# Kernel optimization log

Measured on AMD Instinct MI355X. Metric: run time of the kernel, lower is better.

## Reference

```python
import jax, jax.numpy as jnp
import numpy as np

B, S, D = 1024, 256, 128  # batch, seq_len, emb_dim; concat feat = 4*D = 512
H1, H2 = 256, 64          # att_hidden_size tail; att_hidden_size = [4*D, H1, H2]


def setup_inputs() -> dict:
    key = jax.random.key(0)
    ks = jax.random.split(key, 8)
    queries = jax.random.normal(ks[0], (B, D), dtype=jnp.float32)
    keys = jax.random.normal(ks[1], (B, S, D), dtype=jnp.float32)
    keys_length = jax.random.randint(ks[2], (B,), 1, S + 1)  # in [1, S]
    W1 = jax.random.normal(ks[3], (4 * D, H1), dtype=jnp.float32) * (1.0 / np.sqrt(4 * D))
    b1 = jnp.zeros((H1,), dtype=jnp.float32)
    W2 = jax.random.normal(ks[4], (H1, H2), dtype=jnp.float32) * (1.0 / np.sqrt(H1))
    b2 = jnp.zeros((H2,), dtype=jnp.float32)
    Wd = jax.random.normal(ks[5], (H2, 1), dtype=jnp.float32) * (1.0 / np.sqrt(H2))
    bd = jnp.zeros((1,), dtype=jnp.float32)
    return {"queries": queries, "keys": keys, "keys_length": keys_length,
            "W1": W1, "b1": b1, "W2": W2, "b2": b2, "Wd": Wd, "bd": bd}


def reference(queries, keys, keys_length, W1, b1, W2, b2, Wd, bd):
    # broadcast query across sequence: [B, S, D]
    q = jnp.broadcast_to(queries[:, None, :], keys.shape)
    feat = jnp.concatenate([q, keys, q - keys, q * keys], axis=-1)
    # att MLP (sigmoid after each layer, as in MLPLayers)
    h = jax.nn.sigmoid(jnp.einsum('bsf,fh->bsh', feat, W1) + b1)
    h = jax.nn.sigmoid(jnp.einsum('bsh,hk->bsk', h, W2) + b2)
    score = (jnp.einsum('bsk,ko->bso', h, Wd) + bd)[..., 0]  # [B, S]
    # mask: positions >= keys_length are invalid (mask_mat = arange(S))
    mask = jnp.arange(S)[None, :] >= keys_length[:, None]
    score = jnp.where(mask, -jnp.inf, score)  # softmax_stag=True -> -inf fill
    score = score / jnp.sqrt(jnp.float32(D))
    w = jax.nn.softmax(score, axis=1)  # [B, S]
    # return_seq_weight=False -> weighted sum over keys: [B, 1, D]
    out = jnp.einsum('bs,bsd->bd', w, keys)[:, None, :]
    return out
```

## Files before the change

### kernel.cpp

```cpp
#include <hip/hip_runtime.h>


typedef unsigned short u16;
typedef unsigned int u32;
typedef short bf16x8 __attribute__((ext_vector_type(8)));
typedef float f32x4 __attribute__((ext_vector_type(4)));

#define NBATCH 1024
#define SLEN 256
#define DD 128
#define NH1 256
#define NH2 64

#define WS_WBCT  0
#define WS_WDT   65536
#define WS_W2T   131072
#define WS_WDS   163840
#define WS_WSUM  165888
#define WS_BIAS1 296960

#define L_KBUF   0
#define L_H1     16384
#define L_SCORES 32768
#define L_BIAS   33792
#define L_B2     34816
#define L_WD     35072
#define L_WPART  35344
#define L_RED4   35856
#define L_SIZE   35920

__device__ __forceinline__ u16 f2bf_rne(float f){
  union { float f; unsigned u; } v; v.f = f;
  unsigned r = v.u + 0x7fffu + ((v.u >> 16) & 1u);
  return (u16)(r >> 16);
}
__device__ __forceinline__ u32 pack_trunc(float a, float b){
  return (__float_as_uint(a) >> 16) | (__float_as_uint(b) & 0xffff0000u);
}
__device__ __forceinline__ float b2fl(short s){
  return __uint_as_float(((u32)(u16)s) << 16);
}
__device__ __forceinline__ int swz(int byte){
  return byte ^ (((byte >> 9) & 7) << 4);
}
__device__ __forceinline__ int swzk(int byte){
  return byte ^ (((byte >> 8) & 7) << 4);
}
__device__ __forceinline__ float fsigmoid(float x){
  return __builtin_amdgcn_rcpf(1.f + __expf(-x));
}
__device__ __forceinline__ void barrier_lds(){
  asm volatile("s_waitcnt lgkmcnt(0)" ::: "memory");
  __builtin_amdgcn_s_barrier();
  __builtin_amdgcn_sched_barrier(0);
}

__global__ void prep_weights(const float* __restrict__ W1, const float* __restrict__ W2,
                             const float* __restrict__ Wd, const float* __restrict__ bd,
                             u16* __restrict__ WbcT, u16* __restrict__ WdT,
                             u16* __restrict__ W2T, float* __restrict__ WdS,
                             float* __restrict__ Wsum){
  int n = blockIdx.x;
  int k = threadIdx.x;
  if (k < DD){
    WbcT[n * DD + k] = f2bf_rne(W1[(128 + k) * NH1 + n] - W1[(256 + k) * NH1 + n]);
    WdT [n * DD + k] = f2bf_rne(W1[(384 + k) * NH1 + n]);
    Wsum[k * NH1 + n] = W1[k * NH1 + n] + W1[(256 + k) * NH1 + n];
  }
  if (n < NH2) W2T[n * 256 + k] = f2bf_rne(W2[k * NH2 + n]);
  if (n == 0 && k < NH2) WdS[k] = Wd[k];
  if (n == 0 && k == NH2) WdS[NH2] = bd[0];
}

__global__ void prep_bias(const float* __restrict__ q, const float* __restrict__ Wsum,
                          const float* __restrict__ b1, float* __restrict__ bias1){
  __shared__ float qsh[DD];
  int b = blockIdx.x, j = threadIdx.x;
  if (j < DD) qsh[j] = q[b * DD + j];
  __syncthreads();
  float acc = b1[j];
  #pragma unroll 8
  for (int d = 0; d < DD; ++d)
    acc += qsh[d] * Wsum[d * NH1 + j];
  bias1[b * NH1 + j] = acc;
}

__global__ __launch_bounds__(512, 4)
void seqatt_main(const float* __restrict__ queries, const float* __restrict__ keys,
                 const int* __restrict__ keys_length,
                 const u16* __restrict__ WbcT, const u16* __restrict__ WdT,
                 const u16* __restrict__ W2Tg,
                 const float* __restrict__ WdS, const float* __restrict__ bias1g,
                 const float* __restrict__ b2g, float* __restrict__ out)
{
  __shared__ alignas(16) char smem[L_SIZE];
  float* scores = (float*)(smem + L_SCORES);
  float* bias1s = (float*)(smem + L_BIAS);
  float* b2s    = (float*)(smem + L_B2);
  float* wds    = (float*)(smem + L_WD);
  float* wpart  = (float*)(smem + L_WPART);
  float* red4   = (float*)(smem + L_RED4);

  const int b = blockIdx.x;
  const int tid = threadIdx.x;
  const int lane = tid & 63;
  const int wave = tid >> 6;
  const int l15 = lane & 15;
  const int g   = lane >> 4;
  const int r = tid >> 4, seg = tid & 15;

  if (tid < 256) bias1s[tid] = bias1g[b * NH1 + tid];
  if (tid < 64) b2s[tid] = b2g[tid];
  if (tid < 65) wds[tid] = WdS[tid];
  const int klen = keys_length[b];
  const float* kbb = keys + (long)b * SLEN * DD;

  float4 k0, k1;
#define ISSUE(t) do { const float* p_ = kbb + (((t) << 5) + r) * DD + (seg << 3); \
    k0 = *(const float4*)p_; k1 = *(const float4*)(p_ + 4); } while (0)
#define STORE(t) do { int bb_ = (((t) & 1) << 13) + (r << 8) + (seg << 4); \
    uint4 w_; \
    w_.x = pack_trunc(k0.x, k0.y); w_.y = pack_trunc(k0.z, k0.w); \
    w_.z = pack_trunc(k1.x, k1.y); w_.w = pack_trunc(k1.z, k1.w); \
    *(uint4*)(smem + swzk(bb_)) = w_; } while (0)

  ISSUE(0);

  bf16x8 bfrag[2][4];
  {
    const float* qb = queries + b * DD;
    #pragma unroll
    for (int nt = 0; nt < 2; ++nt){
      int n = (wave << 5) + (nt << 4) + l15;
      #pragma unroll
      for (int kk = 0; kk < 4; ++kk){
        int k0i = (g << 3) + (kk << 5);
        bf16x8 bc = *(const bf16x8*)(WbcT + n * DD + k0i);
        bf16x8 wd = *(const bf16x8*)(WdT  + n * DD + k0i);
        float4 q0 = *(const float4*)(qb + k0i);
        float4 q1 = *(const float4*)(qb + k0i + 4);
        float qa[8] = {q0.x, q0.y, q0.z, q0.w, q1.x, q1.y, q1.z, q1.w};
        union { u16 s[8]; bf16x8 v; } o;
        #pragma unroll
        for (int j = 0; j < 8; ++j)
          o.s[j] = f2bf_rne(fmaf(qa[j], b2fl(wd[j]), b2fl(bc[j])));
        bfrag[nt][kk] = o.v;
      }
    }
  }
  const int sh = wave >> 2;
  const int ob = (wave & 3) << 4;
  bf16x8 w2frag[8];
  #pragma unroll
  for (int kk = 0; kk < 8; ++kk)
    w2frag[kk] = *(const bf16x8*)(W2Tg + (ob + l15) * 256 + (kk << 5) + (g << 3));

  STORE(0);
  barrier_lds();

  const f32x4 fz = {0.f, 0.f, 0.f, 0.f};

  for (int st = 0; st < 8; ++st){
    const int s0 = st << 5;
    const int kb_base = (st & 1) << 13;

    if (st < 7) ISSUE(st + 1);

    f32x4 acc[2][2];
    #pragma unroll
    for (int mt = 0; mt < 2; ++mt)
      #pragma unroll
      for (int nt = 0; nt < 2; ++nt) acc[mt][nt] = fz;
    #pragma unroll
    for (int kk = 0; kk < 4; ++kk){
      bf16x8 af[2];
      #pragma unroll
      for (int mt = 0; mt < 2; ++mt)
        af[mt] = *(const bf16x8*)(smem + swzk(kb_base + (((mt << 4) + l15) << 8) + (kk << 6) + (g << 4)));
      #pragma unroll
      for (int mt = 0; mt < 2; ++mt)
        #pragma unroll
        for (int nt = 0; nt < 2; ++nt)
          acc[mt][nt] = __builtin_amdgcn_mfma_f32_16x16x32_bf16(bfrag[nt][kk], af[mt], acc[mt][nt], 0, 0, 0);
    }

    #pragma unroll
    for (int nt = 0; nt < 2; ++nt){
      float4 bia = *(const float4*)(bias1s + (wave << 5) + (nt << 4) + (g << 2));
      #pragma unroll
      for (int mt = 0; mt < 2; ++mt){
        float v0 = fsigmoid(acc[mt][nt][0] + bia.x);
        float v1 = fsigmoid(acc[mt][nt][1] + bia.y);
        float v2 = fsigmoid(acc[mt][nt][2] + bia.z);
        float v3 = fsigmoid(acc[mt][nt][3] + bia.w);
        uint2 p; p.x = pack_trunc(v0, v1); p.y = pack_trunc(v2, v3);
        int s = (mt << 4) + l15;
        int hb = (wave << 5) + (nt << 4) + (g << 2);
        *(uint2*)(smem + swz(L_H1 + (s << 9) + (hb << 1))) = p;
      }
    }
    barrier_lds();

    f32x4 acc2 = fz;
    #pragma unroll
    for (int kk = 0; kk < 8; ++kk){
      bf16x8 a2 = *(const bf16x8*)(smem + swz(L_H1 + (((sh << 4) + l15) << 9) + (kk << 6) + (g << 4)));
      acc2 = __builtin_amdgcn_mfma_f32_16x16x32_bf16(w2frag[kk], a2, acc2, 0, 0, 0);
    }

    {
      float pp = 0.f;
      #pragma unroll
      for (int i = 0; i < 4; ++i){
        int o = ob + (g << 2) + i;
        pp += fsigmoid(acc2[i] + b2s[o]) * wds[o];
      }
      pp += __shfl_xor(pp, 16); pp += __shfl_xor(pp, 32);
      if (lane < 16)
        wpart[((wave & 3) << 5) + (sh << 4) + l15] = pp;
    }

    if (st < 7) STORE(st + 1);

    barrier_lds();

    if (tid < 32){
      float v = wpart[tid] + wpart[32 + tid] + wpart[64 + tid] + wpart[96 + tid];
      int s = s0 + tid;
      scores[s] = (s < klen) ? (v + wds[64]) * 0.08838834764831845f : -1e30f;
    }
  }

  barrier_lds();

  {
    float v = (tid < 256) ? scores[tid] : -1e30f;
    float m = v;
    #pragma unroll
    for (int off = 32; off >= 1; off >>= 1) m = fmaxf(m, __shfl_xor(m, off));
    if (lane == 0) red4[wave] = m;
    __syncthreads();
    float mx = red4[0];
    #pragma unroll
    for (int w = 1; w < 8; ++w) mx = fmaxf(mx, red4[w]);
    float e = (tid < 256) ? __expf(v - mx) : 0.f;
    float ssum = e;
    #pragma unroll
    for (int off = 32; off >= 1; off >>= 1) ssum += __shfl_xor(ssum, off);
    if (lane == 0) red4[8 + wave] = ssum;
    __syncthreads();
    float tot = 0.f;
    #pragma unroll
    for (int w = 0; w < 8; ++w) tot += red4[8 + w];
    if (tid < 256) scores[tid] = e * __builtin_amdgcn_rcpf(tot);
    __syncthreads();
  }

  {
    float* red = (float*)smem;
    int d = tid & 127, q4 = tid >> 7;
    const float* kb = keys + ((long)b * SLEN + q4 * 64) * DD + d;
    const float* sc = scores + q4 * 64;
    float acc = 0.f;
    #pragma unroll 4
    for (int s2 = 0; s2 < 64; ++s2) acc += sc[s2] * kb[s2 * DD];
    red[tid] = acc;
    __syncthreads();
    if (tid < 128)
      out[b * DD + tid] = (red[tid] + red[128 + tid]) + (red[256 + tid] + red[384 + tid]);
  }
#undef ISSUE
#undef STORE
}

extern "C" void kernel_launch(void* const* d_in, const int* in_sizes, int n_in,
                              void* d_out, int out_size, void* d_ws, size_t ws_size,
                              hipStream_t stream) {
  const float* queries     = (const float*)d_in[0];
  const float* keys        = (const float*)d_in[1];
  const int*   keys_length = (const int*)d_in[2];
  const float* W1 = (const float*)d_in[3];
  const float* b1 = (const float*)d_in[4];
  const float* W2 = (const float*)d_in[5];
  const float* b2 = (const float*)d_in[6];
  const float* Wd = (const float*)d_in[7];
  const float* bd = (const float*)d_in[8];
  float* out = (float*)d_out;
  char* ws = (char*)d_ws;

  u16*   WbcT  = (u16*)(ws + WS_WBCT);
  u16*   WdT   = (u16*)(ws + WS_WDT);
  u16*   W2T   = (u16*)(ws + WS_W2T);
  float* WdS   = (float*)(ws + WS_WDS);
  float* Wsum  = (float*)(ws + WS_WSUM);
  float* bias1 = (float*)(ws + WS_BIAS1);

  prep_weights<<<dim3(256), dim3(256), 0, stream>>>(W1, W2, Wd, bd, WbcT, WdT, W2T, WdS, Wsum);
  prep_bias<<<dim3(NBATCH), dim3(256), 0, stream>>>(queries, Wsum, b1, bias1);
  seqatt_main<<<dim3(NBATCH), dim3(512), 0, stream>>>(queries, keys, keys_length,
                                                      WbcT, WdT, W2T, WdS, bias1, b2, out);
}
```

Baseline: 89.55 us.

## Fuse softmax-weighted key sum into streaming loop using LDS bf16 keys

Keeps three bf16 key tiles in LDS (triple buffering instead of double) so that each tile can be reused after its scores are computed. The weighted sum over keys is accumulated inside the main sequence loop, which removes the second global read of the keys. Softmax no longer subtracts the max: each score is exponentiated directly and the result is divided by the total at the end. The layer-2 MFMA chain is split into two independent accumulators to shorten the dependency chain. In exchange, the output now uses bf16-truncated keys, there is overflow risk if scores become large, and the extra LDS may lower occupancy.

```diff
diff --git a/kernel.cpp b/kernel.cpp
--- a/kernel.cpp
+++ b/kernel.cpp
@@ -20,14 +20,14 @@
 #define WS_BIAS1 296960
 
 #define L_KBUF   0
-#define L_H1     16384
-#define L_SCORES 32768
-#define L_BIAS   33792
-#define L_B2     34816
-#define L_WD     35072
-#define L_WPART  35344
-#define L_RED4   35856
-#define L_SIZE   35920
+#define L_H1     24576
+#define L_SCORES 40960
+#define L_BIAS   41984
+#define L_B2     43008
+#define L_WD     43264
+#define L_WPART  43536
+#define L_RED4   44048
+#define L_SIZE   44112
 
 __device__ __forceinline__ u16 f2bf_rne(float f){
   union { float f; unsigned u; } v; v.f = f;
@@ -108,21 +108,30 @@
   const int l15 = lane & 15;
   const int g   = lane >> 4;
   const int r = tid >> 4, seg = tid & 15;
+  const int dcol = tid & 127, so = (tid >> 7) << 3;
 
   if (tid < 256) bias1s[tid] = bias1g[b * NH1 + tid];
   if (tid < 64) b2s[tid] = b2g[tid];
   if (tid < 65) wds[tid] = WdS[tid];
   const int klen = keys_length[b];
   const float* kbb = keys + (long)b * SLEN * DD;
+  float out_acc = 0.f;
 
   float4 k0, k1;
 #define ISSUE(t) do { const float* p_ = kbb + (((t) << 5) + r) * DD + (seg << 3); \
     k0 = *(const float4*)p_; k1 = *(const float4*)(p_ + 4); } while (0)
-#define STORE(t) do { int bb_ = (((t) & 1) << 13) + (r << 8) + (seg << 4); \
+#define STORE(t) do { int bb_ = ((t) % 3) * 8192 + (r << 8) + (seg << 4); \
     uint4 w_; \
     w_.x = pack_trunc(k0.x, k0.y); w_.y = pack_trunc(k0.z, k0.w); \
     w_.z = pack_trunc(k1.x, k1.y); w_.w = pack_trunc(k1.z, k1.w); \
     *(uint4*)(smem + swzk(bb_)) = w_; } while (0)
+#define ACCUM(t) do { const int kb3_ = ((t) % 3) * 8192; \
+    _Pragma("unroll") \
+    for (int i_ = 0; i_ < 8; ++i_){ \
+      float w_ = scores[((t) << 5) + so + i_]; \
+      u16 kv_ = *(const u16*)(smem + kb3_ + ((so + i_) << 8) + ((dcol << 1) ^ (i_ << 4))); \
+      out_acc = fmaf(w_, b2fl((short)kv_), out_acc); \
+    } } while (0)
 
   ISSUE(0);
 
@@ -160,9 +169,9 @@
 
   const f32x4 fz = {0.f, 0.f, 0.f, 0.f};
 
+  #pragma unroll
   for (int st = 0; st < 8; ++st){
-    const int s0 = st << 5;
-    const int kb_base = (st & 1) << 13;
+    const int kb_base = (st % 3) * 8192;
 
     if (st < 7) ISSUE(st + 1);
 
@@ -201,11 +210,18 @@
     }
     barrier_lds();
 
-    f32x4 acc2 = fz;
-    #pragma unroll
-    for (int kk = 0; kk < 8; ++kk){
+    if (st > 0) ACCUM(st - 1);
+
+    f32x4 acc2a = fz, acc2b = fz;
+    #pragma unroll
+    for (int kk = 0; kk < 4; ++kk){
       bf16x8 a2 = *(const bf16x8*)(smem + swz(L_H1 + (((sh << 4) + l15) << 9) + (kk << 6) + (g << 4)));
-      acc2 = __builtin_amdgcn_mfma_f32_16x16x32_bf16(w2frag[kk], a2, acc2, 0, 0, 0);
+      acc2a = __builtin_amdgcn_mfma_f32_16x16x32_bf16(w2frag[kk], a2, acc2a, 0, 0, 0);
+    }
+    #pragma unroll
+    for (int kk = 4; kk < 8; ++kk){
+      bf16x8 a2 = *(const bf16x8*)(smem + swz(L_H1 + (((sh << 4) + l15) << 9) + (kk << 6) + (g << 4)));
+      acc2b = __builtin_amdgcn_mfma_f32_16x16x32_bf16(w2frag[kk], a2, acc2b, 0, 0, 0);
     }
 
     {
@@ -213,7 +229,7 @@
       #pragma unroll
       for (int i = 0; i < 4; ++i){
         int o = ob + (g << 2) + i;
-        pp += fsigmoid(acc2[i] + b2s[o]) * wds[o];
+        pp += fsigmoid((acc2a[i] + acc2b[i]) + b2s[o]) * wds[o];
       }
       pp += __shfl_xor(pp, 16); pp += __shfl_xor(pp, 32);
       if (lane < 16)
@@ -226,51 +242,37 @@
 
     if (tid < 32){
       float v = wpart[tid] + wpart[32 + tid] + wpart[64 + tid] + wpart[96 + tid];
-      int s = s0 + tid;
-      scores[s] = (s < klen) ? (v + wds[64]) * 0.08838834764831845f : -1e30f;
+      int s = (st << 5) + tid;
+      float sc = (v + wds[64]) * 0.08838834764831845f;
+      scores[s] = (s < klen) ? __expf(sc) : 0.f;
     }
   }
 
   barrier_lds();
-
+  ACCUM(7);
+
+  float tot;
   {
-    float v = (tid < 256) ? scores[tid] : -1e30f;
-    float m = v;
-    #pragma unroll
-    for (int off = 32; off >= 1; off >>= 1) m = fmaxf(m, __shfl_xor(m, off));
-    if (lane == 0) red4[wave] = m;
+    float v = (tid < 256) ? scores[tid] : 0.f;
+    #pragma unroll
+    for (int off = 32; off >= 1; off >>= 1) v += __shfl_xor(v, off);
+    if (lane == 0) red4[wave] = v;
     __syncthreads();
-    float mx = red4[0];
-    #pragma unroll
-    for (int w = 1; w < 8; ++w) mx = fmaxf(mx, red4[w]);
-    float e = (tid < 256) ? __expf(v - mx) : 0.f;
-    float ssum = e;
-    #pragma unroll
-    for (int off = 32; off >= 1; off >>= 1) ssum += __shfl_xor(ssum, off);
-    if (lane == 0) red4[8 + wave] = ssum;
-    __syncthreads();
-    float tot = 0.f;
-    #pragma unroll
-    for (int w = 0; w < 8; ++w) tot += red4[8 + w];
-    if (tid < 256) scores[tid] = e * __builtin_amdgcn_rcpf(tot);
-    __syncthreads();
+    tot = ((red4[0] + red4[1]) + (red4[2] + red4[3])) +
+          ((red4[4] + red4[5]) + (red4[6] + red4[7]));
   }
 
   {
     float* red = (float*)smem;
-    int d = tid & 127, q4 = tid >> 7;
-    const float* kb = keys + ((long)b * SLEN + q4 * 64) * DD + d;
-    const float* sc = scores + q4 * 64;
-    float acc = 0.f;
-    #pragma unroll 4
-    for (int s2 = 0; s2 < 64; ++s2) acc += sc[s2] * kb[s2 * DD];
-    red[tid] = acc;
+    red[tid] = out_acc;
     __syncthreads();
     if (tid < 128)
-      out[b * DD + tid] = (red[tid] + red[128 + tid]) + (red[256 + tid] + red[384 + tid]);
+      out[b * DD + tid] = ((red[tid] + red[128 + tid]) + (red[256 + tid] + red[384 + tid]))
+                          * __builtin_amdgcn_rcpf(tot);
   }
 #undef ISSUE
 #undef STORE
+#undef ACCUM
 }
 
 extern "C" void kernel_launch(void* const* d_in, const int* in_sizes, int n_in,
```

Measured after the change: 210.6 us. 2.35x slower.

## Fold log2e into weights, pad LDS rows instead of XOR swizzle, unroll stage loop

Applied to the files above, without the earlier changes.

Pre-scales W1, W2, the biases and the score scale by log2(e), so the sigmoids and the softmax can use exp2 directly and skip a multiply per exponent. XOR-swizzled LDS addressing is replaced by padded row strides (272 and 528 bytes) with precomputed base offsets. The stage loop is fully unrolled, and the second MFMA chain is split across two accumulators to shorten the dependency chain. This costs somewhat more LDS and code size, and the bf16 rounding of the pre-scaled weights shifts slightly.

```diff
diff --git a/kernel.cpp b/kernel.cpp
--- a/kernel.cpp
+++ b/kernel.cpp
@@ -11,6 +11,7 @@
 #define DD 128
 #define NH1 256
 #define NH2 64
+#define LOG2E 1.4426950408889634f
 
 #define WS_WBCT  0
 #define WS_WDT   65536
@@ -19,15 +20,17 @@
 #define WS_WSUM  165888
 #define WS_BIAS1 296960
 
-#define L_KBUF   0
-#define L_H1     16384
-#define L_SCORES 32768
-#define L_BIAS   33792
-#define L_B2     34816
-#define L_WD     35072
-#define L_WPART  35344
-#define L_RED4   35856
-#define L_SIZE   35920
+#define KROW     272
+#define KBUFSZ   8704
+#define H1ROW    528
+#define L_H1     17408
+#define L_BIAS   34304
+#define L_B2     35328
+#define L_WD     35584
+#define L_WPART  35856
+#define L_SCORES 36368
+#define L_RED4   37392
+#define L_SIZE   37456
 
 __device__ __forceinline__ u16 f2bf_rne(float f){
   union { float f; unsigned u; } v; v.f = f;
@@ -40,14 +43,8 @@
 __device__ __forceinline__ float b2fl(short s){
   return __uint_as_float(((u32)(u16)s) << 16);
 }
-__device__ __forceinline__ int swz(int byte){
-  return byte ^ (((byte >> 9) & 7) << 4);
-}
-__device__ __forceinline__ int swzk(int byte){
-  return byte ^ (((byte >> 8) & 7) << 4);
-}
-__device__ __forceinline__ float fsigmoid(float x){
-  return __builtin_amdgcn_rcpf(1.f + __expf(-x));
+__device__ __forceinline__ float fsig2(float x){
+  return __builtin_amdgcn_rcpf(1.f + exp2f(-x));
 }
 __device__ __forceinline__ void barrier_lds(){
   asm volatile("s_waitcnt lgkmcnt(0)" ::: "memory");
@@ -63,11 +60,11 @@
   int n = blockIdx.x;
   int k = threadIdx.x;
   if (k < DD){
-    WbcT[n * DD + k] = f2bf_rne(W1[(128 + k) * NH1 + n] - W1[(256 + k) * NH1 + n]);
-    WdT [n * DD + k] = f2bf_rne(W1[(384 + k) * NH1 + n]);
-    Wsum[k * NH1 + n] = W1[k * NH1 + n] + W1[(256 + k) * NH1 + n];
-  }
-  if (n < NH2) W2T[n * 256 + k] = f2bf_rne(W2[k * NH2 + n]);
+    WbcT[n * DD + k] = f2bf_rne((W1[(128 + k) * NH1 + n] - W1[(256 + k) * NH1 + n]) * LOG2E);
+    WdT [n * DD + k] = f2bf_rne(W1[(384 + k) * NH1 + n] * LOG2E);
+    Wsum[k * NH1 + n] = (W1[k * NH1 + n] + W1[(256 + k) * NH1 + n]) * LOG2E;
+  }
+  if (n < NH2) W2T[n * 256 + k] = f2bf_rne(W2[k * NH2 + n] * LOG2E);
   if (n == 0 && k < NH2) WdS[k] = Wd[k];
   if (n == 0 && k == NH2) WdS[NH2] = bd[0];
 }
@@ -78,7 +75,7 @@
   int b = blockIdx.x, j = threadIdx.x;
   if (j < DD) qsh[j] = q[b * DD + j];
   __syncthreads();
-  float acc = b1[j];
+  float acc = b1[j] * LOG2E;
   #pragma unroll 8
   for (int d = 0; d < DD; ++d)
     acc += qsh[d] * Wsum[d * NH1 + j];
@@ -94,11 +91,11 @@
                  const float* __restrict__ b2g, float* __restrict__ out)
 {
   __shared__ alignas(16) char smem[L_SIZE];
-  float* scores = (float*)(smem + L_SCORES);
   float* bias1s = (float*)(smem + L_BIAS);
   float* b2s    = (float*)(smem + L_B2);
   float* wds    = (float*)(smem + L_WD);
   float* wpart  = (float*)(smem + L_WPART);
+  float* scores = (float*)(smem + L_SCORES);
   float* red4   = (float*)(smem + L_RED4);
 
   const int b = blockIdx.x;
@@ -110,19 +107,23 @@
   const int r = tid >> 4, seg = tid & 15;
 
   if (tid < 256) bias1s[tid] = bias1g[b * NH1 + tid];
-  if (tid < 64) b2s[tid] = b2g[tid];
+  if (tid < 64) b2s[tid] = b2g[tid] * LOG2E;
   if (tid < 65) wds[tid] = WdS[tid];
   const int klen = keys_length[b];
   const float* kbb = keys + (long)b * SLEN * DD;
 
+  const int a1base = l15 * KROW + (g << 4);
+  const int hwbase = L_H1 + l15 * H1ROW + (((wave << 5) + (g << 2)) << 1);
+  const int stbase = r * KROW + (seg << 4);
+
   float4 k0, k1;
 #define ISSUE(t) do { const float* p_ = kbb + (((t) << 5) + r) * DD + (seg << 3); \
     k0 = *(const float4*)p_; k1 = *(const float4*)(p_ + 4); } while (0)
-#define STORE(t) do { int bb_ = (((t) & 1) << 13) + (r << 8) + (seg << 4); \
+#define STORE(t) do { \
     uint4 w_; \
     w_.x = pack_trunc(k0.x, k0.y); w_.y = pack_trunc(k0.z, k0.w); \
     w_.z = pack_trunc(k1.x, k1.y); w_.w = pack_trunc(k1.z, k1.w); \
-    *(uint4*)(smem + swzk(bb_)) = w_; } while (0)
+    *(uint4*)(smem + (((t) & 1) * KBUFSZ + stbase)) = w_; } while (0)
 
   ISSUE(0);
 
@@ -150,6 +151,7 @@
   }
   const int sh = wave >> 2;
   const int ob = (wave & 3) << 4;
+  const int a2base = L_H1 + ((sh << 4) + l15) * H1ROW + (g << 4);
   bf16x8 w2frag[8];
   #pragma unroll
   for (int kk = 0; kk < 8; ++kk)
@@ -160,9 +162,9 @@
 
   const f32x4 fz = {0.f, 0.f, 0.f, 0.f};
 
+  #pragma unroll
   for (int st = 0; st < 8; ++st){
-    const int s0 = st << 5;
-    const int kb_base = (st & 1) << 13;
+    const int kb_base = (st & 1) * KBUFSZ;
 
     if (st < 7) ISSUE(st + 1);
 
@@ -176,7 +178,7 @@
       bf16x8 af[2];
       #pragma unroll
       for (int mt = 0; mt < 2; ++mt)
-        af[mt] = *(const bf16x8*)(smem + swzk(kb_base + (((mt << 4) + l15) << 8) + (kk << 6) + (g << 4)));
+        af[mt] = *(const bf16x8*)(smem + (kb_base + a1base + mt * 4352 + (kk << 6)));
       #pragma unroll
       for (int mt = 0; mt < 2; ++mt)
         #pragma unroll
@@ -189,23 +191,26 @@
       float4 bia = *(const float4*)(bias1s + (wave << 5) + (nt << 4) + (g << 2));
       #pragma unroll
       for (int mt = 0; mt < 2; ++mt){
-        float v0 = fsigmoid(acc[mt][nt][0] + bia.x);
-        float v1 = fsigmoid(acc[mt][nt][1] + bia.y);
-        float v2 = fsigmoid(acc[mt][nt][2] + bia.z);
-        float v3 = fsigmoid(acc[mt][nt][3] + bia.w);
+        float v0 = fsig2(acc[mt][nt][0] + bia.x);
+        float v1 = fsig2(acc[mt][nt][1] + bia.y);
+        float v2 = fsig2(acc[mt][nt][2] + bia.z);
+        float v3 = fsig2(acc[mt][nt][3] + bia.w);
         uint2 p; p.x = pack_trunc(v0, v1); p.y = pack_trunc(v2, v3);
-        int s = (mt << 4) + l15;
-        int hb = (wave << 5) + (nt << 4) + (g << 2);
-        *(uint2*)(smem + swz(L_H1 + (s << 9) + (hb << 1))) = p;
+        *(uint2*)(smem + (hwbase + mt * 8448 + (nt << 5))) = p;
       }
     }
     barrier_lds();
 
-    f32x4 acc2 = fz;
-    #pragma unroll
-    for (int kk = 0; kk < 8; ++kk){
-      bf16x8 a2 = *(const bf16x8*)(smem + swz(L_H1 + (((sh << 4) + l15) << 9) + (kk << 6) + (g << 4)));
-      acc2 = __builtin_amdgcn_mfma_f32_16x16x32_bf16(w2frag[kk], a2, acc2, 0, 0, 0);
+    f32x4 acc2a = fz, acc2b = fz;
+    #pragma unroll
+    for (int kk = 0; kk < 4; ++kk){
+      bf16x8 a2 = *(const bf16x8*)(smem + (a2base + (kk << 6)));
+      acc2a = __builtin_amdgcn_mfma_f32_16x16x32_bf16(w2frag[kk], a2, acc2a, 0, 0, 0);
+    }
+    #pragma unroll
+    for (int kk = 4; kk < 8; ++kk){
+      bf16x8 a2 = *(const bf16x8*)(smem + (a2base + (kk << 6)));
+      acc2b = __builtin_amdgcn_mfma_f32_16x16x32_bf16(w2frag[kk], a2, acc2b, 0, 0, 0);
     }
 
     {
@@ -213,7 +218,7 @@
       #pragma unroll
       for (int i = 0; i < 4; ++i){
         int o = ob + (g << 2) + i;
-        pp += fsigmoid(acc2[i] + b2s[o]) * wds[o];
+        pp += fsig2((acc2a[i] + acc2b[i]) + b2s[o]) * wds[o];
       }
       pp += __shfl_xor(pp, 16); pp += __shfl_xor(pp, 32);
       if (lane < 16)
@@ -226,8 +231,9 @@
 
     if (tid < 32){
       float v = wpart[tid] + wpart[32 + tid] + wpart[64 + tid] + wpart[96 + tid];
-      int s = s0 + tid;
-      scores[s] = (s < klen) ? (v + wds[64]) * 0.08838834764831845f : -1e30f;
+      int s = (st << 5) + tid;
+      float sc = (v + wds[64]) * 0.12751744692290092f;
+      scores[s] = (s < klen) ? sc : -1e30f;
     }
   }
 
@@ -243,7 +249,7 @@
     float mx = red4[0];
     #pragma unroll
     for (int w = 1; w < 8; ++w) mx = fmaxf(mx, red4[w]);
-    float e = (tid < 256) ? __expf(v - mx) : 0.f;
+    float e = (tid < 256) ? exp2f(v - mx) : 0.f;
     float ssum = e;
     #pragma unroll
     for (int off = 32; off >= 1; off >>= 1) ssum += __shfl_xor(ssum, off);
```

New measurement: 101.9 us (median of 2 runs). +13.8%, slower.

## Triple-buffer keys and double-buffer H1/wpart to drop one barrier per step

Applied to the files above, without the earlier changes.

Keys staging in LDS goes from two to three rotating buffers, and the H1 activations and score partials are double-buffered. This lets the next tile's store and the previous step's score reduction move ahead of the layer-2 MMA, removing one block-wide barrier per sequence step. The layer-2 accumulation is also split into two independent accumulator chains to shorten the MFMA dependency chain. In exchange, LDS use grows from about 35 KB to about 61 KB per block, which may lower occupancy.

```diff
diff --git a/kernel.cpp b/kernel.cpp
--- a/kernel.cpp
+++ b/kernel.cpp
@@ -20,14 +20,14 @@
 #define WS_BIAS1 296960
 
 #define L_KBUF   0
-#define L_H1     16384
-#define L_SCORES 32768
-#define L_BIAS   33792
-#define L_B2     34816
-#define L_WD     35072
-#define L_WPART  35344
-#define L_RED4   35856
-#define L_SIZE   35920
+#define L_H1     24576
+#define L_SCORES 57344
+#define L_BIAS   58368
+#define L_B2     59392
+#define L_WD     59648
+#define L_WPART  59920
+#define L_RED4   60944
+#define L_SIZE   61008
 
 __device__ __forceinline__ u16 f2bf_rne(float f){
   union { float f; unsigned u; } v; v.f = f;
@@ -118,7 +118,7 @@
   float4 k0, k1;
 #define ISSUE(t) do { const float* p_ = kbb + (((t) << 5) + r) * DD + (seg << 3); \
     k0 = *(const float4*)p_; k1 = *(const float4*)(p_ + 4); } while (0)
-#define STORE(t) do { int bb_ = (((t) & 1) << 13) + (r << 8) + (seg << 4); \
+#define STOREB(bufoff) do { int bb_ = (bufoff) + (r << 8) + (seg << 4); \
     uint4 w_; \
     w_.x = pack_trunc(k0.x, k0.y); w_.y = pack_trunc(k0.z, k0.w); \
     w_.z = pack_trunc(k1.x, k1.y); w_.w = pack_trunc(k1.z, k1.w); \
@@ -155,14 +155,14 @@
   for (int kk = 0; kk < 8; ++kk)
     w2frag[kk] = *(const bf16x8*)(W2Tg + (ob + l15) * 256 + (kk << 5) + (g << 3));
 
-  STORE(0);
+  STOREB(0);
   barrier_lds();
 
   const f32x4 fz = {0.f, 0.f, 0.f, 0.f};
+  int kb_cur = 0, kb_nxt = 8192;
 
   for (int st = 0; st < 8; ++st){
-    const int s0 = st << 5;
-    const int kb_base = (st & 1) << 13;
+    const int h_cur = L_H1 + ((st & 1) << 14);
 
     if (st < 7) ISSUE(st + 1);
 
@@ -176,7 +176,7 @@
       bf16x8 af[2];
       #pragma unroll
       for (int mt = 0; mt < 2; ++mt)
-        af[mt] = *(const bf16x8*)(smem + swzk(kb_base + (((mt << 4) + l15) << 8) + (kk << 6) + (g << 4)));
+        af[mt] = *(const bf16x8*)(smem + swzk(kb_cur + (((mt << 4) + l15) << 8) + (kk << 6) + (g << 4)));
       #pragma unroll
       for (int mt = 0; mt < 2; ++mt)
         #pragma unroll
@@ -196,16 +196,32 @@
         uint2 p; p.x = pack_trunc(v0, v1); p.y = pack_trunc(v2, v3);
         int s = (mt << 4) + l15;
         int hb = (wave << 5) + (nt << 4) + (g << 2);
-        *(uint2*)(smem + swz(L_H1 + (s << 9) + (hb << 1))) = p;
+        *(uint2*)(smem + swz(h_cur + (s << 9) + (hb << 1))) = p;
       }
     }
+
+    if (st < 7) STOREB(kb_nxt);
+
     barrier_lds();
 
-    f32x4 acc2 = fz;
-    #pragma unroll
-    for (int kk = 0; kk < 8; ++kk){
-      bf16x8 a2 = *(const bf16x8*)(smem + swz(L_H1 + (((sh << 4) + l15) << 9) + (kk << 6) + (g << 4)));
-      acc2 = __builtin_amdgcn_mfma_f32_16x16x32_bf16(w2frag[kk], a2, acc2, 0, 0, 0);
+    if (st > 0 && tid < 32){
+      const float* wp = wpart + (((st - 1) & 1) << 7);
+      float v = wp[tid] + wp[32 + tid] + wp[64 + tid] + wp[96 + tid];
+      int s = ((st - 1) << 5) + tid;
+      float sc = (v + wds[64]) * 0.08838834764831845f;
+      scores[s] = (s < klen) ? sc : -1e30f;
+    }
+
+    f32x4 acc2a = fz, acc2b = fz;
+    #pragma unroll
+    for (int kk = 0; kk < 4; ++kk){
+      bf16x8 a2 = *(const bf16x8*)(smem + swz(h_cur + (((sh << 4) + l15) << 9) + (kk << 6) + (g << 4)));
+      acc2a = __builtin_amdgcn_mfma_f32_16x16x32_bf16(w2frag[kk], a2, acc2a, 0, 0, 0);
+    }
+    #pragma unroll
+    for (int kk = 4; kk < 8; ++kk){
+      bf16x8 a2 = *(const bf16x8*)(smem + swz(h_cur + (((sh << 4) + l15) << 9) + (kk << 6) + (g << 4)));
+      acc2b = __builtin_amdgcn_mfma_f32_16x16x32_bf16(w2frag[kk], a2, acc2b, 0, 0, 0);
     }
 
     {
@@ -213,24 +229,26 @@
       #pragma unroll
       for (int i = 0; i < 4; ++i){
         int o = ob + (g << 2) + i;
-        pp += fsigmoid(acc2[i] + b2s[o]) * wds[o];
+        pp += fsigmoid((acc2a[i] + acc2b[i]) + b2s[o]) * wds[o];
       }
       pp += __shfl_xor(pp, 16); pp += __shfl_xor(pp, 32);
       if (lane < 16)
-        wpart[((wave & 3) << 5) + (sh << 4) + l15] = pp;
-    }
-
-    if (st < 7) STORE(st + 1);
-
-    barrier_lds();
-
-    if (tid < 32){
-      float v = wpart[tid] + wpart[32 + tid] + wpart[64 + tid] + wpart[96 + tid];
-      int s = s0 + tid;
-      scores[s] = (s < klen) ? (v + wds[64]) * 0.08838834764831845f : -1e30f;
-    }
-  }
-
+        wpart[((st & 1) << 7) + ((wave & 3) << 5) + (sh << 4) + l15] = pp;
+    }
+
+    int t = kb_nxt + 8192;
+    kb_cur = kb_nxt;
+    kb_nxt = (t > 16384) ? 0 : t;
+  }
+
+  barrier_lds();
+  if (tid < 32){
+    const float* wp = wpart + ((7 & 1) << 7);
+    float v = wp[tid] + wp[32 + tid] + wp[64 + tid] + wp[96 + tid];
+    int s = (7 << 5) + tid;
+    float sc = (v + wds[64]) * 0.08838834764831845f;
+    scores[s] = (s < klen) ? sc : -1e30f;
+  }
   barrier_lds();
 
   {
@@ -270,7 +288,7 @@
       out[b * DD + tid] = (red[tid] + red[128 + tid]) + (red[256 + tid] + red[384 + tid]);
   }
 #undef ISSUE
-#undef STORE
+#undef STOREB
 }
 
 extern "C" void kernel_launch(void* const* d_in, const int* in_sizes, int n_in,
```

New measurement: 92.14 us. +2.9%, slower.
